# Kernel optimization log

Hardware: AMD Instinct MI355X
Metric: run time of the kernel (lower is better)

The kernel has to match this reference:

```python
import jax, jax.numpy as jnp
import numpy as np

B, T, H, HEADS, OUT = 16, 8192, 256, 2, 5
PERIOD = 16  # phoneme boundary every 16 frames
EPS_DENOM = 1e-5
LN_EPS = 1e-5
TEMP = 1.0


def setup_inputs() -> dict:
    key = jax.random.key(0)
    ks = jax.random.split(key, 8)
    s = 0.02
    feat = jax.random.normal(ks[0], (B, T, H), jnp.float32)
    ph_bd = jnp.broadcast_to(((jnp.arange(T) % PERIOD) == PERIOD - 1).astype(jnp.int32), (B, T))
    ph_length = T // PERIOD + 1  # 513
    return {
        'feat': feat,
        'ph_bd': ph_bd,
        'ph_length': ph_length,
        'w_attn': jax.random.normal(ks[1], (HEADS, H), jnp.float32) * s,
        'b_attn': jnp.zeros((HEADS,), jnp.float32),
        'ln1_g': jnp.ones((H,), jnp.float32),
        'ln1_b': jnp.zeros((H,), jnp.float32),
        'conv1_w': jax.random.normal(ks[2], (H, H, 3), jnp.float32) * s,
        'conv1_b': jnp.zeros((H,), jnp.float32),
        'conv2_w': jax.random.normal(ks[3], (H, H, 1), jnp.float32) * s,
        'conv2_b': jnp.zeros((H,), jnp.float32),
        'ln2_g': jnp.ones((H,), jnp.float32),
        'ln2_b': jnp.zeros((H,), jnp.float32),
        'post_w': jax.random.normal(ks[4], (H, H, 3), jnp.float32) * s,
        'post_b': jnp.zeros((H,), jnp.float32),
        'w_out': jax.random.normal(ks[5], (OUT, H), jnp.float32) * s,
        'b_out': jnp.zeros((OUT,), jnp.float32),
    }


def _ln_c(x, g, b):
    # LayerNorm over channel dim of [B, C, L]
    m = jnp.mean(x, axis=1, keepdims=True)
    v = jnp.mean((x - m) ** 2, axis=1, keepdims=True)
    return (x - m) * jax.lax.rsqrt(v + LN_EPS) * g[None, :, None] + b[None, :, None]


def _conv1d(x, w, b):
    # x: [B, C, L], w: [O, I, K], 'same' padding
    pad = (w.shape[-1] - 1) // 2
    y = jax.lax.conv_general_dilated(x, w, (1,), [(pad, pad)],
                                     dimension_numbers=('NCH', 'OIH', 'NCH'))
    return y + b[None, :, None]


def reference(feat, ph_bd, ph_length, w_attn, b_attn, ln1_g, ln1_b,
              conv1_w, conv1_b, conv2_w, conv2_b, ln2_g, ln2_b,
              post_w, post_b, w_out, b_out):
    # multihead attention weights per frame: [B, T, heads]
    attn = jax.nn.sigmoid(jnp.einsum('bth,ah->bta', feat, w_attn) + b_attn)
    attn_mean = jnp.mean(attn, axis=-1)                 # [B, T]
    # mean over heads of feat[...,None]*attn == feat * mean(attn)
    attn_feat = feat * attn_mean[..., None]             # [B, T, H]

    mel2ph = jnp.cumsum(ph_bd, axis=1)                  # [B, T] frame->phoneme id
    bidx = jnp.arange(feat.shape[0])[:, None]
    denom = jnp.zeros((feat.shape[0], ph_length), feat.dtype).at[bidx, mel2ph].add(attn_mean)
    ph_agg = jnp.zeros((feat.shape[0], ph_length, feat.shape[2]), feat.dtype).at[bidx, mel2ph].add(attn_feat)
    ph_agg = ph_agg / (denom[..., None] + EPS_DENOM)    # [B, L, H]

    # ConvBlocks (1 residual block, layers_in_block=1, c_multiple=1, swish)
    x = jnp.transpose(ph_agg, (0, 2, 1))                # [B, H, L]
    nonpad = (jnp.sum(jnp.abs(x), axis=1) > 0).astype(x.dtype)[:, None, :]
    h = _ln_c(x, ln1_g, ln1_b)
    h = _conv1d(h, conv1_w, conv1_b) * (3.0 ** -0.5)
    h = jax.nn.silu(h)
    h = _conv1d(h, conv2_w, conv2_b)
    x = (x + h) * nonpad
    x = _ln_c(x, ln2_g, ln2_b) * nonpad
    x = _conv1d(x, post_w, post_b) * nonpad
    out = jnp.transpose(x, (0, 2, 1))                   # [B, L, H]

    tech_logits = (jnp.einsum('blh,oh->blo', out, w_out) + b_out) / TEMP
    return tech_logits
```

## Files before the change

kernel.cpp:

```cpp
#include <hip/hip_runtime.h>
#include <hip/hip_bf16.h>

#define TDIM 8192
#define BDIM 16
#define HDIM 256
#define PHL  513
#define PADL 515
#define MROWS (BDIM*PHL)

typedef __attribute__((ext_vector_type(8))) short  short8;
typedef __attribute__((ext_vector_type(4))) float  floatx4;

__device__ __forceinline__ float sigmoidf_(float x){ return 1.0f/(1.0f+__expf(-x)); }

__device__ __forceinline__ float blk_reduce(float v, float* red){
  #pragma unroll
  for (int off=32; off>0; off>>=1) v += __shfl_xor(v, off, 64);
  int w = threadIdx.x>>6;
  __syncthreads();
  if ((threadIdx.x&63)==0) red[w]=v;
  __syncthreads();
  return red[0]+red[1]+red[2]+red[3];
}

__global__ __launch_bounds__(256) void k_scan(const int* __restrict__ ph_bd,
                                              int* __restrict__ mel2ph){
  int b = blockIdx.x, tid = threadIdx.x;
  const int* in  = ph_bd  + (size_t)b*TDIM;
  int*       out = mel2ph + (size_t)b*TDIM;
  int base = tid*32;
  int vals[32]; int s=0;
  #pragma unroll
  for (int i=0;i<32;i+=4){
    int4 v = *(const int4*)(in+base+i);
    vals[i]=v.x; vals[i+1]=v.y; vals[i+2]=v.z; vals[i+3]=v.w;
    s += v.x+v.y+v.z+v.w;
  }
  __shared__ int ls[256];
  ls[tid]=s; __syncthreads();
  for (int off=1; off<256; off<<=1){
    int t = (tid>=off)? ls[tid-off] : 0;
    __syncthreads();
    ls[tid]+=t;
    __syncthreads();
  }
  int run = ls[tid]-s;
  #pragma unroll
  for (int i=0;i<32;i++){ run += vals[i]; out[base+i]=run; }
}

__global__ __launch_bounds__(256) void k_prep(
    const float* __restrict__ conv1_w, const float* __restrict__ conv2_w,
    const float* __restrict__ post_w,
    __bf16* __restrict__ w1t, __bf16* __restrict__ w2t, __bf16* __restrict__ w3t,
    int* __restrict__ rowoff,
    float* __restrict__ x0pad, __bf16* __restrict__ h1pad, __bf16* __restrict__ x2pad)
{
  int idx = blockIdx.x*256 + threadIdx.x;
  if (idx < 256*768){
    int o = idx/768, j = idx - o*768;
    int dl = j>>8, i = j&255;
    int src = (o*256+i)*3 + dl;
    w1t[idx] = (__bf16)conv1_w[src];
    w3t[idx] = (__bf16)post_w[src];
  }
  if (idx < 256*256)
    w2t[idx] = (__bf16)conv2_w[idx];
  if (idx < MROWS){
    int b = idx/513, l = idx - b*513;
    rowoff[idx] = (b*PADL + l)*HDIM;
  }
  if (idx < BDIM*2*HDIM){
    int b = idx>>9, rr=(idx>>8)&1, c=idx&255;
    size_t row = (size_t)b*PADL + (rr? (PADL-1):0);
    x0pad[row*HDIM+c]=0.f;
    h1pad[row*HDIM+c]=(__bf16)0.f;
    x2pad[row*HDIM+c]=(__bf16)0.f;
  }
}

__global__ __launch_bounds__(256) void k_attn_agg(
    const float* __restrict__ feat, const int* __restrict__ mel2ph,
    const float* __restrict__ w_attn, const float* __restrict__ b_attn,
    const float* __restrict__ ln1_g, const float* __restrict__ ln1_b,
    float* __restrict__ x0pad, __bf16* __restrict__ h1pad, float* __restrict__ nonpad)
{
  int b = blockIdx.x / PHL, p = blockIdx.x - b*PHL;
  int tid = threadIdx.x, lane = tid&63, w = tid>>6;
  __shared__ float sfeat[16][HDIM];
  __shared__ float sam[16];
  __shared__ float red[4];

  const int* row = mel2ph + (size_t)b*TDIM;
  int t0, t1;
  { int lo=0, hi=TDIM; while(lo<hi){ int mid=(lo+hi)>>1; if(row[mid]<p) lo=mid+1; else hi=mid; } t0=lo; }
  { int lo=t0, hi=TDIM; while(lo<hi){ int mid=(lo+hi)>>1; if(row[mid]<p+1) lo=mid+1; else hi=mid; } t1=lo; }

  float wa0[4], wa1[4];
  #pragma unroll
  for (int q=0;q<4;q++){ wa0[q]=w_attn[lane+64*q]; wa1[q]=w_attn[HDIM+lane+64*q]; }
  float ba0=b_attn[0], ba1=b_attn[1];

  float agg=0.f, denom=0.f;
  for (int base=t0; base<t1; base+=16){
    int nf = min(16, t1-base);
    for (int ft=0; ft<nf; ft++)
      sfeat[ft][tid] = feat[((size_t)b*TDIM + base+ft)*HDIM + tid];
    __syncthreads();
    for (int ft=w; ft<nf; ft+=4){
      float d0=0.f, d1=0.f;
      #pragma unroll
      for (int q=0;q<4;q++){ float f=sfeat[ft][lane+64*q]; d0+=f*wa0[q]; d1+=f*wa1[q]; }
      #pragma unroll
      for (int off=32;off>0;off>>=1){ d0+=__shfl_xor(d0,off,64); d1+=__shfl_xor(d1,off,64); }
      if (lane==0) sam[ft] = 0.5f*(sigmoidf_(d0+ba0)+sigmoidf_(d1+ba1));
    }
    __syncthreads();
    for (int ft=0; ft<nf; ft++){ float a=sam[ft]; agg += sfeat[ft][tid]*a; denom += a; }
    __syncthreads();
  }

  float x = agg/(denom+1e-5f);
  float sabs = blk_reduce(fabsf(x), red);
  float np = (sabs>0.f)?1.f:0.f;
  float mean = blk_reduce(x, red)*(1.f/HDIM);
  float d = x-mean;
  float var = blk_reduce(d*d, red)*(1.f/HDIM);
  float h = d*rsqrtf(var+1e-5f)*ln1_g[tid]+ln1_b[tid];

  size_t off = ((size_t)b*PADL + p + 1)*HDIM;
  x0pad[off+tid]=x;
  h1pad[off+tid]=(__bf16)h;
  if (tid==0) nonpad[blockIdx.x]=np;
}

template<int KD, int MODE>
__global__ __launch_bounds__(256) void k_gemm(
    const short* __restrict__ A, const int* __restrict__ rowoff,
    const short* __restrict__ Bt, const float* __restrict__ bias,
    const float* __restrict__ nonpad, void* __restrict__ outp)
{
  __shared__ short As[64][40];
  __shared__ short Bs[64][40];
  int tid = threadIdx.x;
  int m0 = blockIdx.x*64, n0 = blockIdx.y*64;

  int ar  = tid>>2, av8 = (tid&3)*8;
  int am  = m0 + ar;
  bool avalid = am < MROWS;
  const short* aptr;
  if (MODE==1) aptr = A + (size_t)(avalid? am:0)*HDIM;
  else         aptr = A + (avalid? rowoff[am] : 0);
  const short* bptr = Bt + (size_t)(n0 + ar)*KD;

  int lane=tid&63, w=tid>>6;
  int wm=(w>>1)*32, wn=(w&1)*32, quad=lane>>4, l15=lane&15;

  floatx4 acc[2][2] = {};
  for (int k0=0;k0<KD;k0+=32){
    short8 a8 = {0,0,0,0,0,0,0,0};
    if (avalid) a8 = *(const short8*)(aptr + k0 + av8);
    short8 b8 = *(const short8*)(bptr + k0 + av8);
    __syncthreads();
    *(short8*)&As[ar][av8] = a8;
    *(short8*)&Bs[ar][av8] = b8;
    __syncthreads();
    short8 af[2], bfr[2];
    #pragma unroll
    for (int t=0;t<2;t++){
      af[t]  = *(const short8*)&As[wm + t*16 + l15][quad*8];
      bfr[t] = *(const short8*)&Bs[wn + t*16 + l15][quad*8];
    }
    #pragma unroll
    for (int ti=0;ti<2;ti++)
      #pragma unroll
      for (int tj=0;tj<2;tj++)
        acc[ti][tj] = __builtin_amdgcn_mfma_f32_16x16x32_bf16(af[ti], bfr[tj], acc[ti][tj], 0,0,0);
  }
  #pragma unroll
  for (int ti=0;ti<2;ti++){
    int mb = m0 + wm + ti*16 + quad*4;
    #pragma unroll
    for (int tj=0;tj<2;tj++){
      int n = n0 + wn + tj*16 + l15;
      #pragma unroll
      for (int r=0;r<4;r++){
        int mm = mb + r;
        if (mm < MROWS){
          float v = acc[ti][tj][r] + bias[n];
          if (MODE==0){
            v *= 0.57735026918962576f;
            v  = v * sigmoidf_(v);
            ((__bf16*)outp)[(size_t)mm*HDIM+n] = (__bf16)v;
          } else if (MODE==1){
            ((float*)outp)[(size_t)mm*HDIM+n] = v;
          } else {
            v *= nonpad[mm];
            ((__bf16*)outp)[(size_t)mm*HDIM+n] = (__bf16)v;
          }
        }
      }
    }
  }
}

__global__ __launch_bounds__(256) void k_resid_ln2(
    const float* __restrict__ x0pad, const float* __restrict__ h2,
    const int* __restrict__ rowoff, const float* __restrict__ nonpad,
    const float* __restrict__ g2, const float* __restrict__ b2,
    __bf16* __restrict__ x2pad)
{
  __shared__ float red[4];
  int r = blockIdx.x, tid = threadIdx.x;
  int off = rowoff[r] + HDIM;
  float np = nonpad[r];
  float x = (x0pad[off+tid] + h2[(size_t)r*HDIM+tid]) * np;
  float mean = blk_reduce(x, red)*(1.f/HDIM);
  float d = x-mean;
  float var = blk_reduce(d*d, red)*(1.f/HDIM);
  x2pad[off+tid] = (__bf16)((d*rsqrtf(var+1e-5f)*g2[tid]+b2[tid])*np);
}

__global__ __launch_bounds__(256) void k_logits(
    const __bf16* __restrict__ outb, const float* __restrict__ w_out,
    const float* __restrict__ b_out, float* __restrict__ dst)
{
  int r = blockIdx.x*4 + (threadIdx.x>>6);
  int lane = threadIdx.x & 63;
  float x[4];
  #pragma unroll
  for (int q=0;q<4;q++) x[q] = (float)outb[(size_t)r*HDIM + lane + 64*q];
  float p[5];
  #pragma unroll
  for (int o=0;o<5;o++){
    float s=0.f;
    #pragma unroll
    for (int q=0;q<4;q++) s += x[q]*w_out[o*HDIM+lane+64*q];
    #pragma unroll
    for (int off=32;off>0;off>>=1) s += __shfl_xor(s,off,64);
    p[o]=s;
  }
  if (lane==0){
    #pragma unroll
    for (int o=0;o<5;o++) dst[(size_t)r*5+o] = p[o] + b_out[o];
  }
}

extern "C" void kernel_launch(void* const* d_in, const int* in_sizes, int n_in,
                              void* d_out, int out_size, void* d_ws, size_t ws_size,
                              hipStream_t stream) {
  const float* feat    = (const float*)d_in[0];
  const int*   ph_bd   = (const int*)  d_in[1];
  const float* w_attn  = (const float*)d_in[3];
  const float* b_attn  = (const float*)d_in[4];
  const float* ln1_g   = (const float*)d_in[5];
  const float* ln1_b   = (const float*)d_in[6];
  const float* conv1_w = (const float*)d_in[7];
  const float* conv1_b = (const float*)d_in[8];
  const float* conv2_w = (const float*)d_in[9];
  const float* conv2_b = (const float*)d_in[10];
  const float* ln2_g   = (const float*)d_in[11];
  const float* ln2_b   = (const float*)d_in[12];
  const float* post_w  = (const float*)d_in[13];
  const float* post_b  = (const float*)d_in[14];
  const float* w_out   = (const float*)d_in[15];
  const float* b_out   = (const float*)d_in[16];

  char* wp = (char*)d_ws;
  auto alloc = [&](size_t bytes)->void*{
    void* p = (void*)wp; wp += (bytes + 255) & ~(size_t)255; return p;
  };
  int*    mel2ph = (int*)   alloc((size_t)BDIM*TDIM*4);
  int*    rowoff = (int*)   alloc((size_t)MROWS*4);
  float*  x0pad  = (float*) alloc((size_t)BDIM*PADL*HDIM*4);
  __bf16* h1pad  = (__bf16*)alloc((size_t)BDIM*PADL*HDIM*2);
  __bf16* g      = (__bf16*)alloc((size_t)MROWS*HDIM*2);
  float*  h2     = (float*) alloc((size_t)MROWS*HDIM*4);
  __bf16* x2pad  = (__bf16*)alloc((size_t)BDIM*PADL*HDIM*2);
  __bf16* outb   = (__bf16*)alloc((size_t)MROWS*HDIM*2);
  float*  nonpad = (float*) alloc((size_t)MROWS*4);
  __bf16* w1t    = (__bf16*)alloc((size_t)256*768*2);
  __bf16* w2t    = (__bf16*)alloc((size_t)256*256*2);
  __bf16* w3t    = (__bf16*)alloc((size_t)256*768*2);

  k_scan<<<BDIM, 256, 0, stream>>>(ph_bd, mel2ph);
  k_prep<<<768, 256, 0, stream>>>(conv1_w, conv2_w, post_w, w1t, w2t, w3t,
                                  rowoff, x0pad, h1pad, x2pad);
  k_attn_agg<<<MROWS, 256, 0, stream>>>(feat, mel2ph, w_attn, b_attn,
                                        ln1_g, ln1_b, x0pad, h1pad, nonpad);
  dim3 gg(129, 4);
  k_gemm<768,0><<<gg, 256, 0, stream>>>((const short*)h1pad, rowoff, (const short*)w1t,
                                        conv1_b, nullptr, (void*)g);
  k_gemm<256,1><<<gg, 256, 0, stream>>>((const short*)g, rowoff, (const short*)w2t,
                                        conv2_b, nullptr, (void*)h2);
  k_resid_ln2<<<MROWS, 256, 0, stream>>>(x0pad, h2, rowoff, nonpad, ln2_g, ln2_b, x2pad);
  k_gemm<768,2><<<gg, 256, 0, stream>>>((const short*)x2pad, rowoff, (const short*)w3t,
                                        post_b, nonpad, (void*)outb);
  k_logits<<<MROWS/4, 256, 0, stream>>>(outb, w_out, b_out, (float*)d_out);
}
```

Before: 290.2 us.

## Fuse conv GEMMs with LN2 and logits, replace binary search with segment table

The scan kernel now writes per-phoneme segment start indices, so the attention kernel reads its frame range directly instead of running two binary searches. The attention kernel loads features as float4. Conv1, SiLU and conv2 plus residual and LayerNorm2 are fused into one kernel that keeps the intermediate in LDS, and the post conv is fused with the output projection. Both fused kernels use direct global-to-LDS loads and 64x256 tiles. This removes intermediate global round-trips and several launches, but leaves only 129 blocks per GEMM kernel, which underfills the GPU.

```diff
diff --git a/kernel.cpp b/kernel.cpp
--- a/kernel.cpp
+++ b/kernel.cpp
@@ -7,11 +7,18 @@
 #define PHL  513
 #define PADL 515
 #define MROWS (BDIM*PHL)
+#define SEGW 514
 
 typedef __attribute__((ext_vector_type(8))) short  short8;
 typedef __attribute__((ext_vector_type(4))) float  floatx4;
 
 __device__ __forceinline__ float sigmoidf_(float x){ return 1.0f/(1.0f+__expf(-x)); }
+
+typedef __attribute__((address_space(1))) const unsigned int gu32;
+typedef __attribute__((address_space(3))) unsigned int lu32;
+__device__ __forceinline__ void g2l16(const void* g, void* l){
+  __builtin_amdgcn_global_load_lds((gu32*)g, (lu32*)l, 16, 0, 0);
+}
 
 __device__ __forceinline__ float blk_reduce(float v, float* red){
   #pragma unroll
@@ -24,10 +31,10 @@
 }
 
 __global__ __launch_bounds__(256) void k_scan(const int* __restrict__ ph_bd,
-                                              int* __restrict__ mel2ph){
+                                              int* __restrict__ seg){
   int b = blockIdx.x, tid = threadIdx.x;
-  const int* in  = ph_bd  + (size_t)b*TDIM;
-  int*       out = mel2ph + (size_t)b*TDIM;
+  const int* in = ph_bd + (size_t)b*TDIM;
+  int sb = b*SEGW;
   int base = tid*32;
   int vals[32]; int s=0;
   #pragma unroll
@@ -44,9 +51,15 @@
     ls[tid]+=t;
     __syncthreads();
   }
-  int run = ls[tid]-s;
-  #pragma unroll
-  for (int i=0;i<32;i++){ run += vals[i]; out[base+i]=run; }
+  int cur = ls[tid]-s;
+  #pragma unroll
+  for (int i=0;i<32;i++){
+    int nxt = cur + vals[i];
+    for (int v=cur+1; v<=nxt; v++) seg[sb+v] = base+i;
+    cur = nxt;
+  }
+  if (tid==0) seg[sb] = 0;
+  if (tid==255){ for (int v=cur+1; v<SEGW; v++) seg[sb+v] = TDIM; }
 }
 
 __global__ __launch_bounds__(256) void k_prep(
@@ -79,44 +92,41 @@
   }
 }
 
-__global__ __launch_bounds__(256) void k_attn_agg(
-    const float* __restrict__ feat, const int* __restrict__ mel2ph,
+__global__ __launch_bounds__(256) void k_attn(
+    const float* __restrict__ feat, const int* __restrict__ seg,
     const float* __restrict__ w_attn, const float* __restrict__ b_attn,
     const float* __restrict__ ln1_g, const float* __restrict__ ln1_b,
     float* __restrict__ x0pad, __bf16* __restrict__ h1pad, float* __restrict__ nonpad)
 {
   int b = blockIdx.x / PHL, p = blockIdx.x - b*PHL;
   int tid = threadIdx.x, lane = tid&63, w = tid>>6;
-  __shared__ float sfeat[16][HDIM];
+  __shared__ float4 sfeat[16*64];
   __shared__ float sam[16];
   __shared__ float red[4];
 
-  const int* row = mel2ph + (size_t)b*TDIM;
-  int t0, t1;
-  { int lo=0, hi=TDIM; while(lo<hi){ int mid=(lo+hi)>>1; if(row[mid]<p) lo=mid+1; else hi=mid; } t0=lo; }
-  { int lo=t0, hi=TDIM; while(lo<hi){ int mid=(lo+hi)>>1; if(row[mid]<p+1) lo=mid+1; else hi=mid; } t1=lo; }
-
-  float wa0[4], wa1[4];
-  #pragma unroll
-  for (int q=0;q<4;q++){ wa0[q]=w_attn[lane+64*q]; wa1[q]=w_attn[HDIM+lane+64*q]; }
-  float ba0=b_attn[0], ba1=b_attn[1];
+  int t0 = seg[b*SEGW + p], t1 = seg[b*SEGW + p + 1];
+
+  float4 wa0 = ((const float4*)w_attn)[lane];
+  float4 wa1 = ((const float4*)(w_attn+HDIM))[lane];
+  float ba0 = b_attn[0], ba1 = b_attn[1];
 
   float agg=0.f, denom=0.f;
   for (int base=t0; base<t1; base+=16){
     int nf = min(16, t1-base);
-    for (int ft=0; ft<nf; ft++)
-      sfeat[ft][tid] = feat[((size_t)b*TDIM + base+ft)*HDIM + tid];
+    const float4* src = (const float4*)(feat + ((size_t)b*TDIM + base)*HDIM);
+    for (int idx=tid; idx<nf*64; idx+=256) sfeat[idx] = src[idx];
     __syncthreads();
     for (int ft=w; ft<nf; ft+=4){
-      float d0=0.f, d1=0.f;
-      #pragma unroll
-      for (int q=0;q<4;q++){ float f=sfeat[ft][lane+64*q]; d0+=f*wa0[q]; d1+=f*wa1[q]; }
+      float4 f = sfeat[ft*64+lane];
+      float d0 = f.x*wa0.x + f.y*wa0.y + f.z*wa0.z + f.w*wa0.w;
+      float d1 = f.x*wa1.x + f.y*wa1.y + f.z*wa1.z + f.w*wa1.w;
       #pragma unroll
       for (int off=32;off>0;off>>=1){ d0+=__shfl_xor(d0,off,64); d1+=__shfl_xor(d1,off,64); }
       if (lane==0) sam[ft] = 0.5f*(sigmoidf_(d0+ba0)+sigmoidf_(d1+ba1));
     }
     __syncthreads();
-    for (int ft=0; ft<nf; ft++){ float a=sam[ft]; agg += sfeat[ft][tid]*a; denom += a; }
+    const float* sf = (const float*)sfeat;
+    for (int ft=0; ft<nf; ft++){ float a=sam[ft]; agg += sf[ft*HDIM+tid]*a; denom += a; }
     __syncthreads();
   }
 
@@ -134,115 +144,196 @@
   if (tid==0) nonpad[blockIdx.x]=np;
 }
 
-template<int KD, int MODE>
-__global__ __launch_bounds__(256) void k_gemm(
-    const short* __restrict__ A, const int* __restrict__ rowoff,
-    const short* __restrict__ Bt, const float* __restrict__ bias,
-    const float* __restrict__ nonpad, void* __restrict__ outp)
-{
-  __shared__ short As[64][40];
-  __shared__ short Bs[64][40];
-  int tid = threadIdx.x;
-  int m0 = blockIdx.x*64, n0 = blockIdx.y*64;
-
-  int ar  = tid>>2, av8 = (tid&3)*8;
-  int am  = m0 + ar;
-  bool avalid = am < MROWS;
-  const short* aptr;
-  if (MODE==1) aptr = A + (size_t)(avalid? am:0)*HDIM;
-  else         aptr = A + (avalid? rowoff[am] : 0);
-  const short* bptr = Bt + (size_t)(n0 + ar)*KD;
-
-  int lane=tid&63, w=tid>>6;
-  int wm=(w>>1)*32, wn=(w&1)*32, quad=lane>>4, l15=lane&15;
-
-  floatx4 acc[2][2] = {};
-  for (int k0=0;k0<KD;k0+=32){
-    short8 a8 = {0,0,0,0,0,0,0,0};
-    if (avalid) a8 = *(const short8*)(aptr + k0 + av8);
-    short8 b8 = *(const short8*)(bptr + k0 + av8);
-    __syncthreads();
-    *(short8*)&As[ar][av8] = a8;
-    *(short8*)&Bs[ar][av8] = b8;
-    __syncthreads();
-    short8 af[2], bfr[2];
-    #pragma unroll
-    for (int t=0;t<2;t++){
-      af[t]  = *(const short8*)&As[wm + t*16 + l15][quad*8];
-      bfr[t] = *(const short8*)&Bs[wn + t*16 + l15][quad*8];
-    }
-    #pragma unroll
-    for (int ti=0;ti<2;ti++)
-      #pragma unroll
-      for (int tj=0;tj<2;tj++)
-        acc[ti][tj] = __builtin_amdgcn_mfma_f32_16x16x32_bf16(af[ti], bfr[tj], acc[ti][tj], 0,0,0);
-  }
-  #pragma unroll
-  for (int ti=0;ti<2;ti++){
-    int mb = m0 + wm + ti*16 + quad*4;
-    #pragma unroll
-    for (int tj=0;tj<2;tj++){
-      int n = n0 + wn + tj*16 + l15;
-      #pragma unroll
-      for (int r=0;r<4;r++){
-        int mm = mb + r;
-        if (mm < MROWS){
-          float v = acc[ti][tj][r] + bias[n];
-          if (MODE==0){
-            v *= 0.57735026918962576f;
-            v  = v * sigmoidf_(v);
-            ((__bf16*)outp)[(size_t)mm*HDIM+n] = (__bf16)v;
-          } else if (MODE==1){
-            ((float*)outp)[(size_t)mm*HDIM+n] = v;
-          } else {
-            v *= nonpad[mm];
-            ((__bf16*)outp)[(size_t)mm*HDIM+n] = (__bf16)v;
-          }
-        }
-      }
-    }
-  }
-}
-
-__global__ __launch_bounds__(256) void k_resid_ln2(
-    const float* __restrict__ x0pad, const float* __restrict__ h2,
-    const int* __restrict__ rowoff, const float* __restrict__ nonpad,
+__global__ __launch_bounds__(256) void k_convblock(
+    const short* __restrict__ h1pad, const int* __restrict__ rowoff,
+    const short* __restrict__ w1t, const short* __restrict__ w2t,
+    const float* __restrict__ c1b, const float* __restrict__ c2b,
+    const float* __restrict__ x0pad, const float* __restrict__ nonpad,
     const float* __restrict__ g2, const float* __restrict__ b2,
     __bf16* __restrict__ x2pad)
 {
-  __shared__ float red[4];
-  int r = blockIdx.x, tid = threadIdx.x;
-  int off = rowoff[r] + HDIM;
-  float np = nonpad[r];
-  float x = (x0pad[off+tid] + h2[(size_t)r*HDIM+tid]) * np;
-  float mean = blk_reduce(x, red)*(1.f/HDIM);
-  float d = x-mean;
-  float var = blk_reduce(d*d, red)*(1.f/HDIM);
-  x2pad[off+tid] = (__bf16)((d*rsqrtf(var+1e-5f)*g2[tid]+b2[tid])*np);
-}
-
-__global__ __launch_bounds__(256) void k_logits(
-    const __bf16* __restrict__ outb, const float* __restrict__ w_out,
+  __shared__ __align__(16) short As[4*64*8];
+  __shared__ __align__(16) short Bs[4*256*8];
+  __shared__ __align__(16) short Gt[32*64*8];
+  int tid=threadIdx.x, lane=tid&63, w=tid>>6, quad=lane>>4, l15=lane&15;
+  int m0 = blockIdx.x*64;
+  int am = min(m0 + lane, MROWS-1);
+  const short* aRow = h1pad + rowoff[am];
+  short* AsW = &As[w*64*8];
+
+  floatx4 acc[16];
+  #pragma unroll
+  for (int i=0;i<16;i++) acc[i] = (floatx4){0.f,0.f,0.f,0.f};
+
+  for (int chunk=0; chunk<24; chunk++){
+    int k0 = chunk*32;
+    g2l16(aRow + k0 + w*8, AsW);
+    #pragma unroll
+    for (int ng=0; ng<4; ng++)
+      g2l16(w1t + (size_t)(ng*64+lane)*768 + k0 + w*8, &Bs[(w*256 + ng*64)*8]);
+    __syncthreads();
+    short8 af = *(const short8*)&As[(quad*64 + w*16 + l15)*8];
+    #pragma unroll
+    for (int nt=0; nt<16; nt++){
+      short8 bf = *(const short8*)&Bs[(quad*256 + nt*16 + l15)*8];
+      acc[nt] = __builtin_amdgcn_mfma_f32_16x16x32_bf16(af, bf, acc[nt], 0,0,0);
+    }
+    __syncthreads();
+  }
+
+  const float inv_s3 = 0.57735026918962576f;
+  #pragma unroll
+  for (int nt=0; nt<16; nt++){
+    int n = nt*16 + l15;
+    float bias = c1b[n];
+    #pragma unroll
+    for (int r=0;r<4;r++){
+      float v = (acc[nt][r] + bias)*inv_s3;
+      v = v*sigmoidf_(v);
+      int ml = w*16 + quad*4 + r;
+      ((__bf16*)Gt)[((n>>3)*64 + ml)*8 + (n&7)] = (__bf16)v;
+    }
+  }
+
+  floatx4 acc2[16];
+  #pragma unroll
+  for (int i=0;i<16;i++) acc2[i] = (floatx4){0.f,0.f,0.f,0.f};
+  for (int chunk=0; chunk<8; chunk++){
+    int k0 = chunk*32;
+    #pragma unroll
+    for (int ng=0; ng<4; ng++)
+      g2l16(w2t + (size_t)(ng*64+lane)*256 + k0 + w*8, &Bs[(w*256 + ng*64)*8]);
+    __syncthreads();
+    short8 af = *(const short8*)&Gt[((chunk*4+quad)*64 + w*16 + l15)*8];
+    #pragma unroll
+    for (int nt=0; nt<16; nt++){
+      short8 bf = *(const short8*)&Bs[(quad*256 + nt*16 + l15)*8];
+      acc2[nt] = __builtin_amdgcn_mfma_f32_16x16x32_bf16(af, bf, acc2[nt], 0,0,0);
+    }
+    __syncthreads();
+  }
+
+  int mbase = m0 + w*16 + quad*4;
+  float np_[4]; const float* x0b[4]; int roff[4];
+  #pragma unroll
+  for (int r=0;r<4;r++){
+    int m = min(mbase + r, MROWS-1);
+    np_[r] = nonpad[m];
+    roff[r] = rowoff[m] + HDIM;
+    x0b[r] = x0pad + roff[r];
+  }
+  float sum[4]={0,0,0,0}, ssq[4]={0,0,0,0};
+  #pragma unroll
+  for (int nt=0; nt<16; nt++){
+    int n = nt*16 + l15;
+    float cb = c2b[n];
+    #pragma unroll
+    for (int r=0;r<4;r++){
+      float x = (x0b[r][n] + acc2[nt][r] + cb)*np_[r];
+      acc2[nt][r] = x;
+      sum[r]+=x; ssq[r]+=x*x;
+    }
+  }
+  #pragma unroll
+  for (int off=1; off<16; off<<=1){
+    #pragma unroll
+    for (int r=0;r<4;r++){ sum[r]+=__shfl_xor(sum[r],off,64); ssq[r]+=__shfl_xor(ssq[r],off,64); }
+  }
+  float mean[4], rs[4];
+  #pragma unroll
+  for (int r=0;r<4;r++){
+    mean[r]=sum[r]*(1.f/HDIM);
+    float var=ssq[r]*(1.f/HDIM)-mean[r]*mean[r];
+    rs[r]=rsqrtf(var+1e-5f);
+  }
+  #pragma unroll
+  for (int nt=0; nt<16; nt++){
+    int n = nt*16 + l15;
+    float gg=g2[n], bb=b2[n];
+    #pragma unroll
+    for (int r=0;r<4;r++){
+      int m = mbase + r;
+      if (m < MROWS){
+        float y = ((acc2[nt][r]-mean[r])*rs[r]*gg + bb)*np_[r];
+        x2pad[roff[r]+n] = (__bf16)y;
+      }
+    }
+  }
+}
+
+__global__ __launch_bounds__(256) void k_post(
+    const short* __restrict__ x2pad, const int* __restrict__ rowoff,
+    const short* __restrict__ w3t, const float* __restrict__ postb,
+    const float* __restrict__ nonpad, const float* __restrict__ w_out,
     const float* __restrict__ b_out, float* __restrict__ dst)
 {
-  int r = blockIdx.x*4 + (threadIdx.x>>6);
-  int lane = threadIdx.x & 63;
-  float x[4];
-  #pragma unroll
-  for (int q=0;q<4;q++) x[q] = (float)outb[(size_t)r*HDIM + lane + 64*q];
-  float p[5];
-  #pragma unroll
-  for (int o=0;o<5;o++){
-    float s=0.f;
-    #pragma unroll
-    for (int q=0;q<4;q++) s += x[q]*w_out[o*HDIM+lane+64*q];
-    #pragma unroll
-    for (int off=32;off>0;off>>=1) s += __shfl_xor(s,off,64);
-    p[o]=s;
-  }
-  if (lane==0){
-    #pragma unroll
-    for (int o=0;o<5;o++) dst[(size_t)r*5+o] = p[o] + b_out[o];
+  __shared__ __align__(16) short As[4*64*8];
+  __shared__ __align__(16) short Bs[4*256*8];
+  __shared__ float ws[5*256];
+  int tid=threadIdx.x, lane=tid&63, w=tid>>6, quad=lane>>4, l15=lane&15;
+  int m0 = blockIdx.x*64;
+  int am = min(m0 + lane, MROWS-1);
+  const short* aRow = x2pad + rowoff[am];
+  short* AsW = &As[w*64*8];
+  for (int i=tid; i<5*256; i+=256) ws[i]=w_out[i];
+
+  floatx4 acc[16];
+  #pragma unroll
+  for (int i=0;i<16;i++) acc[i] = (floatx4){0.f,0.f,0.f,0.f};
+  for (int chunk=0; chunk<24; chunk++){
+    int k0 = chunk*32;
+    g2l16(aRow + k0 + w*8, AsW);
+    #pragma unroll
+    for (int ng=0; ng<4; ng++)
+      g2l16(w3t + (size_t)(ng*64+lane)*768 + k0 + w*8, &Bs[(w*256 + ng*64)*8]);
+    __syncthreads();
+    short8 af = *(const short8*)&As[(quad*64 + w*16 + l15)*8];
+    #pragma unroll
+    for (int nt=0; nt<16; nt++){
+      short8 bf = *(const short8*)&Bs[(quad*256 + nt*16 + l15)*8];
+      acc[nt] = __builtin_amdgcn_mfma_f32_16x16x32_bf16(af, bf, acc[nt], 0,0,0);
+    }
+    __syncthreads();
+  }
+
+  int mbase = m0 + w*16 + quad*4;
+  float np_[4];
+  #pragma unroll
+  for (int r=0;r<4;r++) np_[r] = nonpad[min(mbase+r, MROWS-1)];
+  float p[4][5];
+  #pragma unroll
+  for (int r=0;r<4;r++)
+    #pragma unroll
+    for (int o=0;o<5;o++) p[r][o]=0.f;
+  #pragma unroll
+  for (int nt=0; nt<16; nt++){
+    int n = nt*16 + l15;
+    float pb = postb[n];
+    float wv[5];
+    #pragma unroll
+    for (int o=0;o<5;o++) wv[o]=ws[o*256+n];
+    #pragma unroll
+    for (int r=0;r<4;r++){
+      float v = (acc[nt][r] + pb)*np_[r];
+      #pragma unroll
+      for (int o=0;o<5;o++) p[r][o] += v*wv[o];
+    }
+  }
+  #pragma unroll
+  for (int off=1; off<16; off<<=1)
+    #pragma unroll
+    for (int r=0;r<4;r++)
+      #pragma unroll
+      for (int o=0;o<5;o++) p[r][o]+=__shfl_xor(p[r][o],off,64);
+  if (l15==0){
+    #pragma unroll
+    for (int r=0;r<4;r++){
+      int m = mbase + r;
+      if (m < MROWS){
+        #pragma unroll
+        for (int o=0;o<5;o++) dst[(size_t)m*5+o] = p[r][o] + b_out[o];
+      }
+    }
   }
 }
 
@@ -270,31 +361,24 @@
   auto alloc = [&](size_t bytes)->void*{
     void* p = (void*)wp; wp += (bytes + 255) & ~(size_t)255; return p;
   };
-  int*    mel2ph = (int*)   alloc((size_t)BDIM*TDIM*4);
+  int*    seg    = (int*)   alloc((size_t)BDIM*SEGW*4);
   int*    rowoff = (int*)   alloc((size_t)MROWS*4);
   float*  x0pad  = (float*) alloc((size_t)BDIM*PADL*HDIM*4);
   __bf16* h1pad  = (__bf16*)alloc((size_t)BDIM*PADL*HDIM*2);
-  __bf16* g      = (__bf16*)alloc((size_t)MROWS*HDIM*2);
-  float*  h2     = (float*) alloc((size_t)MROWS*HDIM*4);
   __bf16* x2pad  = (__bf16*)alloc((size_t)BDIM*PADL*HDIM*2);
-  __bf16* outb   = (__bf16*)alloc((size_t)MROWS*HDIM*2);
   float*  nonpad = (float*) alloc((size_t)MROWS*4);
   __bf16* w1t    = (__bf16*)alloc((size_t)256*768*2);
   __bf16* w2t    = (__bf16*)alloc((size_t)256*256*2);
   __bf16* w3t    = (__bf16*)alloc((size_t)256*768*2);
 
-  k_scan<<<BDIM, 256, 0, stream>>>(ph_bd, mel2ph);
+  k_scan<<<BDIM, 256, 0, stream>>>(ph_bd, seg);
   k_prep<<<768, 256, 0, stream>>>(conv1_w, conv2_w, post_w, w1t, w2t, w3t,
                                   rowoff, x0pad, h1pad, x2pad);
-  k_attn_agg<<<MROWS, 256, 0, stream>>>(feat, mel2ph, w_attn, b_attn,
-                                        ln1_g, ln1_b, x0pad, h1pad, nonpad);
-  dim3 gg(129, 4);
-  k_gemm<768,0><<<gg, 256, 0, stream>>>((const short*)h1pad, rowoff, (const short*)w1t,
-                                        conv1_b, nullptr, (void*)g);
-  k_gemm<256,1><<<gg, 256, 0, stream>>>((const short*)g, rowoff, (const short*)w2t,
-                                        conv2_b, nullptr, (void*)h2);
-  k_resid_ln2<<<MROWS, 256, 0, stream>>>(x0pad, h2, rowoff, nonpad, ln2_g, ln2_b, x2pad);
-  k_gemm<768,2><<<gg, 256, 0, stream>>>((const short*)x2pad, rowoff, (const short*)w3t,
-                                        post_b, nonpad, (void*)outb);
-  k_logits<<<MROWS/4, 256, 0, stream>>>(outb, w_out, b_out, (float*)d_out);
-}
+  k_attn<<<MROWS, 256, 0, stream>>>(feat, seg, w_attn, b_attn,
+                                    ln1_g, ln1_b, x0pad, h1pad, nonpad);
+  k_convblock<<<129, 256, 0, stream>>>((const short*)h1pad, rowoff, (const short*)w1t,
+                                       (const short*)w2t, conv1_b, conv2_b,
+                                       x0pad, nonpad, ln2_g, ln2_b, x2pad);
+  k_post<<<129, 256, 0, stream>>>((const short*)x2pad, rowoff, (const short*)w3t,
+                                  post_b, nonpad, w_out, b_out, (float*)d_out);
+}
```

After: 309.7 us. +6.7%, slower.
